# Kernel tuning notes

Measured on AMD Instinct MI355X. Metric: run time of the kernel, lower is better.

The kernel has to match this reference:

```python
import jax, jax.numpy as jnp
import numpy as np

D_MODEL = 1024
N_HEADS = 16
HEAD_DIM = D_MODEL // N_HEADS
SCALE = HEAD_DIM ** -0.5
BATCH = 4
SEQ = 2048


def setup_inputs() -> dict:
    key = jax.random.key(0)
    k_x, k_wqkv, k_bqkv, k_wo, k_bo = jax.random.split(key, 5)
    x = jax.random.normal(k_x, (BATCH, SEQ, D_MODEL), dtype=jnp.float32)
    # causal mask: True = masked (matches torch masked_fill semantics)
    mask = jnp.triu(jnp.ones((SEQ, SEQ), dtype=bool), k=1)
    # Linear params (stored as [in, out] for x @ W)
    lim_qkv = (1.0 / D_MODEL) ** 0.5
    W_qkv = jax.random.uniform(k_wqkv, (D_MODEL, 3 * D_MODEL), jnp.float32, -lim_qkv, lim_qkv)
    b_qkv = jax.random.uniform(k_bqkv, (3 * D_MODEL,), jnp.float32, -lim_qkv, lim_qkv)
    W_out = jax.random.uniform(k_wo, (D_MODEL, D_MODEL), jnp.float32, -lim_qkv, lim_qkv)
    b_out = jax.random.uniform(k_bo, (D_MODEL,), jnp.float32, -lim_qkv, lim_qkv)
    return {"x": x, "mask": mask, "W_qkv": W_qkv, "b_qkv": b_qkv, "W_out": W_out, "b_out": b_out}


def reference(x, mask, W_qkv, b_qkv, W_out, b_out):
    b, s, d = x.shape
    qkv = x @ W_qkv + b_qkv                      # [b, s, 3d]
    qkv = qkv.reshape(b, s, 3, N_HEADS, HEAD_DIM)
    qkv = jnp.transpose(qkv, (2, 0, 3, 1, 4))    # [3, b, h, s, hd]
    q, k, v = qkv[0], qkv[1], qkv[2]
    scores = jnp.einsum('bhqd,bhkd->bhqk', q, k) * SCALE  # [b, h, s, s]
    scores = jnp.where(mask[None, None, :, :], -jnp.inf, scores)
    weights = jax.nn.softmax(scores, axis=-1)
    out = jnp.einsum('bhqk,bhkd->bhqd', weights, v)       # [b, h, s, hd]
    out = jnp.transpose(out, (0, 2, 1, 3)).reshape(b, s, d)
    return out @ W_out + b_out
```

## Files before the change

### kernel.cpp

```cpp
#include <hip/hip_runtime.h>

#define BATCH 4
#define SEQ 2048
#define DM 1024
#define NH 16
#define SCALE 0.125f

typedef unsigned short ushort_t;
typedef short bf16x8 __attribute__((ext_vector_type(8)));
typedef float f32x4 __attribute__((ext_vector_type(4)));

__device__ __forceinline__ ushort_t f2bf(float f) {
    unsigned u = __float_as_uint(f);
    unsigned r = (u + 0x7FFFu + ((u >> 16) & 1u)) >> 16;
    return (ushort_t)r;
}

__device__ __forceinline__ unsigned cvtpk_bf16(float lo, float hi) {
    unsigned r;
    asm("v_cvt_pk_bf16_f32 %0, %1, %2" : "=v"(r) : "v"(lo), "v"(hi));
    return r;
}

__device__ __forceinline__ void glds16(const ushort_t* g, ushort_t* l) {
    __builtin_amdgcn_global_load_lds(
        (const __attribute__((address_space(1))) unsigned*)g,
        (__attribute__((address_space(3))) unsigned*)l, 16, 0, 0);
}

__global__ void cast_f32_bf16(const float* __restrict__ in, ushort_t* __restrict__ out, int n) {
    int i = (blockIdx.x * blockDim.x + threadIdx.x) * 4;
    if (i < n) {
        float4 v = *(const float4*)(in + i);
        ushort4 o;
        o.x = f2bf(v.x); o.y = f2bf(v.y); o.z = f2bf(v.z); o.w = f2bf(v.w);
        *(ushort4*)(out + i) = o;
    }
}

__global__ void transpose_cast(const float* __restrict__ in, ushort_t* __restrict__ out,
                               int K, int N) {
    __shared__ float tile[32][33];
    int n0 = blockIdx.x * 32, k0 = blockIdx.y * 32;
    int x = threadIdx.x, y = threadIdx.y;
#pragma unroll
    for (int j = 0; j < 32; j += 8)
        tile[y + j][x] = in[(size_t)(k0 + y + j) * N + n0 + x];
    __syncthreads();
#pragma unroll
    for (int j = 0; j < 32; j += 8)
        out[(size_t)(n0 + y + j) * K + k0 + x] = f2bf(tile[x][y + j]);
}

template <bool OUT_F32>
__global__ __launch_bounds__(256) void gemm_abt(
    const ushort_t* __restrict__ A, const ushort_t* __restrict__ Bt,
    const float* __restrict__ bias, void* __restrict__ Cout,
    int M, int N, int K) {
    __shared__ __attribute__((aligned(16))) ushort_t As[128 * 64];
    __shared__ __attribute__((aligned(16))) ushort_t Bs[128 * 64];
    const int tid = threadIdx.x;
    const int lane = tid & 63, wave = tid >> 6;
    const int l15 = lane & 15, l4 = lane >> 4;
    const int m0 = blockIdx.y * 128, n0 = blockIdx.x * 128;
    const int wr = (wave >> 1) * 64, wc = (wave & 1) * 64;
    const int r8 = lane >> 3;
    const int kch = (lane & 7) ^ r8;
    const ushort_t* gA = A + (size_t)(m0 + wave * 32 + r8) * K + kch * 8;
    const ushort_t* gB = Bt + (size_t)(n0 + wave * 32 + r8) * K + kch * 8;
    const int r7 = l15 & 7;

    f32x4 acc[4][4];
#pragma unroll
    for (int i = 0; i < 4; ++i)
#pragma unroll
        for (int j = 0; j < 4; ++j) acc[i][j] = (f32x4){0.f, 0.f, 0.f, 0.f};

    for (int k0 = 0; k0 < K; k0 += 64) {
#pragma unroll
        for (int c = 0; c < 4; ++c) {
            glds16(gA + k0 + (size_t)(c * 8) * K, &As[(wave * 32 + c * 8) * 64]);
            glds16(gB + k0 + (size_t)(c * 8) * K, &Bs[(wave * 32 + c * 8) * 64]);
        }
        __syncthreads();
#pragma unroll
        for (int kh = 0; kh < 2; ++kh) {
            const int ch = ((kh * 4 + l4) ^ r7) * 8;
            bf16x8 a[4], b[4];
#pragma unroll
            for (int i = 0; i < 4; ++i) {
                a[i] = *(const bf16x8*)&As[(wr + i * 16 + l15) * 64 + ch];
                b[i] = *(const bf16x8*)&Bs[(wc + i * 16 + l15) * 64 + ch];
            }
#pragma unroll
            for (int mi = 0; mi < 4; ++mi)
#pragma unroll
                for (int ni = 0; ni < 4; ++ni)
                    acc[mi][ni] = __builtin_amdgcn_mfma_f32_16x16x32_bf16(
                        a[mi], b[ni], acc[mi][ni], 0, 0, 0);
        }
        __syncthreads();
    }

#pragma unroll
    for (int mi = 0; mi < 4; ++mi)
#pragma unroll
        for (int ni = 0; ni < 4; ++ni)
#pragma unroll
            for (int r = 0; r < 4; ++r) {
                int row = m0 + wr + mi * 16 + l4 * 4 + r;
                int col = n0 + wc + ni * 16 + l15;
                float v = acc[mi][ni][r] + bias[col];
                if (OUT_F32)
                    ((float*)Cout)[(size_t)row * N + col] = v;
                else
                    ((ushort_t*)Cout)[(size_t)row * N + col] = f2bf(v);
            }
}

struct AState {
    bf16x8 q0, q1;
    f32x4 o[4];
    float m, l;
};

__device__ __forceinline__ void scatterV(ushort_t* V, bf16x8 v0, bf16x8 v1, int key, int d0) {
#pragma unroll
    for (int j = 0; j < 8; ++j) {
        int d = d0 + j;
        V[d * 64 + (key ^ ((d & 7) << 3))] = (ushort_t)v0[j];
        int d2 = d0 + 8 + j;
        V[d2 * 64 + (key ^ ((d2 & 7) << 3))] = (ushort_t)v1[j];
    }
}

#define EXPC 0.18033688011112042f

__device__ __forceinline__ void attn_tile(AState& S, const ushort_t* __restrict__ Ks,
                                          const ushort_t* __restrict__ Vt,
                                          ushort_t* __restrict__ Plw,
                                          int l15, int l4, int rel) {
    float p[16];
    float pmax = -INFINITY;
    __builtin_amdgcn_s_setprio(1);
#pragma unroll
    for (int kt = 0; kt < 4; ++kt) {
        const int row = kt * 16 + l15, r7 = row & 7;
        bf16x8 ak0 = *(const bf16x8*)&Ks[row * 64 + ((l4 ^ r7) * 8)];
        bf16x8 ak1 = *(const bf16x8*)&Ks[row * 64 + (((4 + l4) ^ r7) * 8)];
        f32x4 z = {0.f, 0.f, 0.f, 0.f};
        z = __builtin_amdgcn_mfma_f32_16x16x32_bf16(ak0, S.q0, z, 0, 0, 0);
        z = __builtin_amdgcn_mfma_f32_16x16x32_bf16(ak1, S.q1, z, 0, 0, 0);
#pragma unroll
        for (int r = 0; r < 4; ++r) {
            float v = (kt * 16 + l4 * 4 + r > rel) ? -INFINITY : z[r];
            p[kt * 4 + r] = v;
            pmax = fmaxf(pmax, v);
        }
    }
    __builtin_amdgcn_s_setprio(0);
    pmax = fmaxf(pmax, __shfl_xor(pmax, 16));
    pmax = fmaxf(pmax, __shfl_xor(pmax, 32));

    const bool defer = __all(pmax - S.m <= 64.f);
    const float mref = defer ? S.m : fmaxf(S.m, pmax);
    const float mC = mref * EXPC;
    float rsum = 0.f;
#pragma unroll
    for (int i = 0; i < 16; ++i) {
        p[i] = __builtin_exp2f(fmaf(p[i], EXPC, -mC));
        rsum += p[i];
    }
    rsum += __shfl_xor(rsum, 16);
    rsum += __shfl_xor(rsum, 32);
    if (defer) {
        S.l += rsum;
    } else {
        const float scl = __builtin_exp2f((S.m - mref) * EXPC);
        S.l = S.l * scl + rsum;
        S.m = mref;
        const float sc0 = __shfl(scl, l4 * 4 + 0);
        const float sc1 = __shfl(scl, l4 * 4 + 1);
        const float sc2 = __shfl(scl, l4 * 4 + 2);
        const float sc3 = __shfl(scl, l4 * 4 + 3);
#pragma unroll
        for (int dt = 0; dt < 4; ++dt) {
            S.o[dt][0] *= sc0; S.o[dt][1] *= sc1; S.o[dt][2] *= sc2; S.o[dt][3] *= sc3;
        }
    }

    const int pr7 = l15 & 7;
#pragma unroll
    for (int kt = 0; kt < 4; ++kt) {
        uint2 w;
        w.x = cvtpk_bf16(p[kt * 4 + 0], p[kt * 4 + 1]);
        w.y = cvtpk_bf16(p[kt * 4 + 2], p[kt * 4 + 3]);
        *(uint2*)&Plw[l15 * 64 + ((kt * 16 + l4 * 4) ^ (pr7 << 3))] = w;
    }

    bf16x8 pa0 = *(const bf16x8*)&Plw[l15 * 64 + ((l4 ^ pr7) * 8)];
    bf16x8 pa1 = *(const bf16x8*)&Plw[l15 * 64 + (((4 + l4) ^ pr7) * 8)];
    __builtin_amdgcn_s_setprio(1);
#pragma unroll
    for (int dt = 0; dt < 4; ++dt) {
        const int d = dt * 16 + l15, r7 = d & 7;
        bf16x8 bv0 = *(const bf16x8*)&Vt[d * 64 + ((l4 ^ r7) * 8)];
        bf16x8 bv1 = *(const bf16x8*)&Vt[d * 64 + (((4 + l4) ^ r7) * 8)];
        S.o[dt] = __builtin_amdgcn_mfma_f32_16x16x32_bf16(pa0, bv0, S.o[dt], 0, 0, 0);
        S.o[dt] = __builtin_amdgcn_mfma_f32_16x16x32_bf16(pa1, bv1, S.o[dt], 0, 0, 0);
    }
    __builtin_amdgcn_s_setprio(0);
}

__device__ __forceinline__ void process_qblock(
    int bq, const ushort_t* __restrict__ qkv, ushort_t* __restrict__ out,
    size_t rowbase, int h, int wave, int l15, int l4,
    const ushort_t* gk, const ushort_t* gv, int sv_key, int sv_d0,
    ushort_t* Ks0, ushort_t* Ks1, ushort_t* Vt0, ushort_t* Vt1, ushort_t* Plw) {
    const int qbase = bq * 64 + wave * 16;

    AState S;
    {
        const ushort_t* qp = qkv + (rowbase + qbase + l15) * 3072 + h * 64 + l4 * 8;
        S.q0 = *(const bf16x8*)qp;
        S.q1 = *(const bf16x8*)(qp + 32);
    }
#pragma unroll
    for (int i = 0; i < 4; ++i) S.o[i] = (f32x4){0.f, 0.f, 0.f, 0.f};
    S.m = -INFINITY;
    S.l = 0.f;

    glds16(gk, &Ks0[(wave * 16) * 64]);
    glds16(gk + (size_t)8 * 3072, &Ks0[(wave * 16 + 8) * 64]);
    {
        bf16x8 v0 = *(const bf16x8*)gv;
        bf16x8 v1 = *(const bf16x8*)(gv + 8);
        scatterV(Vt0, v0, v1, sv_key, sv_d0);
    }
    __syncthreads();

    const int nt = bq + 1;
    for (int t = 0; t < nt; ++t) {
        ushort_t* Kc = (t & 1) ? Ks1 : Ks0;
        ushort_t* Vc = (t & 1) ? Vt1 : Vt0;
        ushort_t* Kn = (t & 1) ? Ks0 : Ks1;
        ushort_t* Vn = (t & 1) ? Vt0 : Vt1;
        const bool more = (t + 1 < nt);
        bf16x8 nv0, nv1;
        if (more) {
            const size_t koff = (size_t)(t + 1) * 64 * 3072;
            glds16(gk + koff, &Kn[(wave * 16) * 64]);
            glds16(gk + koff + (size_t)8 * 3072, &Kn[(wave * 16 + 8) * 64]);
            nv0 = *(const bf16x8*)(gv + koff);
            nv1 = *(const bf16x8*)(gv + koff + 8);
        }
        attn_tile(S, Kc, Vc, Plw, l15, l4, qbase + l15 - t * 64);
        if (more)
            scatterV(Vn, nv0, nv1, sv_key, sv_d0);
        __syncthreads();
    }

    const float li0 = __shfl(S.l, l4 * 4 + 0);
    const float li1 = __shfl(S.l, l4 * 4 + 1);
    const float li2 = __shfl(S.l, l4 * 4 + 2);
    const float li3 = __shfl(S.l, l4 * 4 + 3);
#pragma unroll
    for (int r = 0; r < 4; ++r) {
        const int qr = qbase + l4 * 4 + r;
        const float li = (r == 0) ? li0 : (r == 1) ? li1 : (r == 2) ? li2 : li3;
        ushort_t* op = out + (rowbase + qr) * DM + h * 64 + l15;
#pragma unroll
        for (int dt = 0; dt < 4; ++dt)
            op[dt * 16] = f2bf(S.o[dt][r] / li);
    }
}

__global__ __launch_bounds__(256, 4) void attn_kernel(const ushort_t* __restrict__ qkv,
                                                      ushort_t* __restrict__ out) {
    __shared__ __attribute__((aligned(16))) ushort_t Ks[2][64 * 64];
    __shared__ __attribute__((aligned(16))) ushort_t Vt[2][64 * 64];
    __shared__ __attribute__((aligned(16))) ushort_t Pl[4][16 * 64];
    const int tid = threadIdx.x;
    const int wave = tid >> 6, lane = tid & 63;
    const int l15 = lane & 15, l4 = lane >> 4;
    const int bh = blockIdx.x;
    const int b = bh >> 4, h = bh & 15;
    const int pair = blockIdx.y;
    const size_t rowbase = (size_t)b * SEQ;

    const int krow = lane >> 3;
    const int kch = (lane & 7) ^ krow;
    const int sv_key = tid & 63, sv_d0 = (tid >> 6) * 16;
    const ushort_t* gk = qkv + (rowbase + wave * 16 + krow) * 3072 + 1024 + h * 64 + kch * 8;
    const ushort_t* gv = qkv + (rowbase + sv_key) * 3072 + 2048 + h * 64 + sv_d0;

    process_qblock(31 - pair, qkv, out, rowbase, h, wave, l15, l4,
                   gk, gv, sv_key, sv_d0, Ks[0], Ks[1], Vt[0], Vt[1], Pl[wave]);
    process_qblock(pair, qkv, out, rowbase, h, wave, l15, l4,
                   gk, gv, sv_key, sv_d0, Ks[0], Ks[1], Vt[0], Vt[1], Pl[wave]);
}

extern "C" void kernel_launch(void* const* d_in, const int* in_sizes, int n_in,
                              void* d_out, int out_size, void* d_ws, size_t ws_size,
                              hipStream_t stream) {
    const float* x     = (const float*)d_in[0];
    const float* W_qkv = (const float*)d_in[2];
    const float* b_qkv = (const float*)d_in[3];
    const float* W_out = (const float*)d_in[4];
    const float* b_out = (const float*)d_in[5];
    float* out = (float*)d_out;

    char* ws = (char*)d_ws;
    ushort_t* xb    = (ushort_t*)(ws);
    ushort_t* WqkvT = (ushort_t*)(ws + 16777216);
    ushort_t* WoutT = (ushort_t*)(ws + 23068672);
    ushort_t* qkv   = (ushort_t*)(ws + 25165824);
    ushort_t* attn  = (ushort_t*)(ws + 75497472);

    const int nx = BATCH * SEQ * DM;
    cast_f32_bf16<<<nx / (256 * 4), 256, 0, stream>>>(x, xb, nx);
    transpose_cast<<<dim3(3 * DM / 32, DM / 32), dim3(32, 8), 0, stream>>>(W_qkv, WqkvT, DM, 3 * DM);
    transpose_cast<<<dim3(DM / 32, DM / 32), dim3(32, 8), 0, stream>>>(W_out, WoutT, DM, DM);

    gemm_abt<false><<<dim3(3 * DM / 128, BATCH * SEQ / 128), 256, 0, stream>>>(
        xb, WqkvT, b_qkv, qkv, BATCH * SEQ, 3 * DM, DM);

    attn_kernel<<<dim3(BATCH * NH, SEQ / 128), 256, 0, stream>>>(qkv, attn);

    gemm_abt<true><<<dim3(DM / 128, BATCH * SEQ / 128), 256, 0, stream>>>(
        attn, WoutT, b_out, out, BATCH * SEQ, DM, DM);
}
```

Before: 289.8 us.

## Emit transposed V from QKV GEMM epilogue and async-load it in attention

The QKV GEMM now writes Q and K to a packed [tokens, 2048] buffer and V in a per-batch transposed [head_dim, seq] layout straight from its epilogue. The attention kernel can then stage V tiles with the same async global-to-LDS copies used for K, replacing the per-element register scatter into LDS. The causal mask is also specialized so only the diagonal tile pays for the mask compare. The cost is strided 8-byte stores in the V epilogue of the GEMM.

```diff
diff --git a/kernel.cpp b/kernel.cpp
--- a/kernel.cpp
+++ b/kernel.cpp
@@ -52,10 +52,91 @@
         out[(size_t)(n0 + y + j) * K + k0 + x] = f2bf(tile[x][y + j]);
 }
 
-template <bool OUT_F32>
+
+__global__ __launch_bounds__(256) void gemm_qkv(
+    const ushort_t* __restrict__ A, const ushort_t* __restrict__ Bt,
+    const float* __restrict__ bias, ushort_t* __restrict__ qk,
+    ushort_t* __restrict__ vt, int M, int N, int K) {
+    __shared__ __attribute__((aligned(16))) ushort_t As[128 * 64];
+    __shared__ __attribute__((aligned(16))) ushort_t Bs[128 * 64];
+    const int tid = threadIdx.x;
+    const int lane = tid & 63, wave = tid >> 6;
+    const int l15 = lane & 15, l4 = lane >> 4;
+    const int m0 = blockIdx.y * 128, n0 = blockIdx.x * 128;
+    const int wr = (wave >> 1) * 64, wc = (wave & 1) * 64;
+    const int r8 = lane >> 3;
+    const int kch = (lane & 7) ^ r8;
+    const ushort_t* gA = A + (size_t)(m0 + wave * 32 + r8) * K + kch * 8;
+    const ushort_t* gB = Bt + (size_t)(n0 + wave * 32 + r8) * K + kch * 8;
+    const int r7 = l15 & 7;
+
+    f32x4 acc[4][4];
+#pragma unroll
+    for (int i = 0; i < 4; ++i)
+#pragma unroll
+        for (int j = 0; j < 4; ++j) acc[i][j] = (f32x4){0.f, 0.f, 0.f, 0.f};
+
+    for (int k0 = 0; k0 < K; k0 += 64) {
+#pragma unroll
+        for (int c = 0; c < 4; ++c) {
+            glds16(gA + k0 + (size_t)(c * 8) * K, &As[(wave * 32 + c * 8) * 64]);
+            glds16(gB + k0 + (size_t)(c * 8) * K, &Bs[(wave * 32 + c * 8) * 64]);
+        }
+        __syncthreads();
+#pragma unroll
+        for (int kh = 0; kh < 2; ++kh) {
+            const int ch = ((kh * 4 + l4) ^ r7) * 8;
+            bf16x8 a[4], b[4];
+#pragma unroll
+            for (int i = 0; i < 4; ++i) {
+                a[i] = *(const bf16x8*)&As[(wr + i * 16 + l15) * 64 + ch];
+                b[i] = *(const bf16x8*)&Bs[(wc + i * 16 + l15) * 64 + ch];
+            }
+#pragma unroll
+            for (int mi = 0; mi < 4; ++mi)
+#pragma unroll
+                for (int ni = 0; ni < 4; ++ni)
+                    acc[mi][ni] = __builtin_amdgcn_mfma_f32_16x16x32_bf16(
+                        a[mi], b[ni], acc[mi][ni], 0, 0, 0);
+        }
+        __syncthreads();
+    }
+
+    if (n0 < 2048) {
+#pragma unroll
+        for (int mi = 0; mi < 4; ++mi)
+#pragma unroll
+            for (int ni = 0; ni < 4; ++ni) {
+                const int col = n0 + wc + ni * 16 + l15;
+                const float bv = bias[col];
+#pragma unroll
+                for (int r = 0; r < 4; ++r) {
+                    const int row = m0 + wr + mi * 16 + l4 * 4 + r;
+                    qk[(size_t)row * 2048 + col] = f2bf(acc[mi][ni][r] + bv);
+                }
+            }
+    } else {
+#pragma unroll
+        for (int mi = 0; mi < 4; ++mi)
+#pragma unroll
+            for (int ni = 0; ni < 4; ++ni) {
+                const int hdg = n0 + wc + ni * 16 + l15 - 2048;
+                const float bv = bias[2048 + hdg];
+                const int row0 = m0 + wr + mi * 16 + l4 * 4;
+                const int bb = row0 >> 11, s0 = row0 & 2047;
+                ushort4 pk;
+                pk.x = f2bf(acc[mi][ni][0] + bv);
+                pk.y = f2bf(acc[mi][ni][1] + bv);
+                pk.z = f2bf(acc[mi][ni][2] + bv);
+                pk.w = f2bf(acc[mi][ni][3] + bv);
+                *(ushort4*)&vt[((size_t)bb * 1024 + hdg) * 2048 + s0] = pk;
+            }
+    }
+}
+
 __global__ __launch_bounds__(256) void gemm_abt(
     const ushort_t* __restrict__ A, const ushort_t* __restrict__ Bt,
-    const float* __restrict__ bias, void* __restrict__ Cout,
+    const float* __restrict__ bias, float* __restrict__ Cout,
     int M, int N, int K) {
     __shared__ __attribute__((aligned(16))) ushort_t As[128 * 64];
     __shared__ __attribute__((aligned(16))) ushort_t Bs[128 * 64];
@@ -108,13 +189,9 @@
         for (int ni = 0; ni < 4; ++ni)
 #pragma unroll
             for (int r = 0; r < 4; ++r) {
-                int row = m0 + wr + mi * 16 + l4 * 4 + r;
-                int col = n0 + wc + ni * 16 + l15;
-                float v = acc[mi][ni][r] + bias[col];
-                if (OUT_F32)
-                    ((float*)Cout)[(size_t)row * N + col] = v;
-                else
-                    ((ushort_t*)Cout)[(size_t)row * N + col] = f2bf(v);
+                const int row = m0 + wr + mi * 16 + l4 * 4 + r;
+                const int col = n0 + wc + ni * 16 + l15;
+                Cout[(size_t)row * N + col] = acc[mi][ni][r] + bias[col];
             }
 }
 
@@ -124,18 +201,9 @@
     float m, l;
 };
 
-__device__ __forceinline__ void scatterV(ushort_t* V, bf16x8 v0, bf16x8 v1, int key, int d0) {
-#pragma unroll
-    for (int j = 0; j < 8; ++j) {
-        int d = d0 + j;
-        V[d * 64 + (key ^ ((d & 7) << 3))] = (ushort_t)v0[j];
-        int d2 = d0 + 8 + j;
-        V[d2 * 64 + (key ^ ((d2 & 7) << 3))] = (ushort_t)v1[j];
-    }
-}
-
 #define EXPC 0.18033688011112042f
 
+template <bool MASK>
 __device__ __forceinline__ void attn_tile(AState& S, const ushort_t* __restrict__ Ks,
                                           const ushort_t* __restrict__ Vt,
                                           ushort_t* __restrict__ Plw,
@@ -153,7 +221,8 @@
         z = __builtin_amdgcn_mfma_f32_16x16x32_bf16(ak1, S.q1, z, 0, 0, 0);
 #pragma unroll
         for (int r = 0; r < 4; ++r) {
-            float v = (kt * 16 + l4 * 4 + r > rel) ? -INFINITY : z[r];
+            float v = z[r];
+            if (MASK) v = (kt * 16 + l4 * 4 + r > rel) ? -INFINITY : v;
             p[kt * 4 + r] = v;
             pmax = fmaxf(pmax, v);
         }
@@ -213,15 +282,15 @@
 }
 
 __device__ __forceinline__ void process_qblock(
-    int bq, const ushort_t* __restrict__ qkv, ushort_t* __restrict__ out,
+    int bq, const ushort_t* __restrict__ qk, ushort_t* __restrict__ out,
     size_t rowbase, int h, int wave, int l15, int l4,
-    const ushort_t* gk, const ushort_t* gv, int sv_key, int sv_d0,
+    const ushort_t* gk, const ushort_t* gvt,
     ushort_t* Ks0, ushort_t* Ks1, ushort_t* Vt0, ushort_t* Vt1, ushort_t* Plw) {
     const int qbase = bq * 64 + wave * 16;
 
     AState S;
     {
-        const ushort_t* qp = qkv + (rowbase + qbase + l15) * 3072 + h * 64 + l4 * 8;
+        const ushort_t* qp = qk + (rowbase + qbase + l15) * 2048 + h * 64 + l4 * 8;
         S.q0 = *(const bf16x8*)qp;
         S.q1 = *(const bf16x8*)(qp + 32);
     }
@@ -231,12 +300,9 @@
     S.l = 0.f;
 
     glds16(gk, &Ks0[(wave * 16) * 64]);
-    glds16(gk + (size_t)8 * 3072, &Ks0[(wave * 16 + 8) * 64]);
-    {
-        bf16x8 v0 = *(const bf16x8*)gv;
-        bf16x8 v1 = *(const bf16x8*)(gv + 8);
-        scatterV(Vt0, v0, v1, sv_key, sv_d0);
-    }
+    glds16(gk + (size_t)8 * 2048, &Ks0[(wave * 16 + 8) * 64]);
+    glds16(gvt, &Vt0[(wave * 16) * 64]);
+    glds16(gvt + (size_t)8 * 2048, &Vt0[(wave * 16 + 8) * 64]);
     __syncthreads();
 
     const int nt = bq + 1;
@@ -245,18 +311,18 @@
         ushort_t* Vc = (t & 1) ? Vt1 : Vt0;
         ushort_t* Kn = (t & 1) ? Ks0 : Ks1;
         ushort_t* Vn = (t & 1) ? Vt0 : Vt1;
-        const bool more = (t + 1 < nt);
-        bf16x8 nv0, nv1;
-        if (more) {
-            const size_t koff = (size_t)(t + 1) * 64 * 3072;
+        if (t + 1 < nt) {
+            const size_t koff = (size_t)(t + 1) * 64 * 2048;
             glds16(gk + koff, &Kn[(wave * 16) * 64]);
-            glds16(gk + koff + (size_t)8 * 3072, &Kn[(wave * 16 + 8) * 64]);
-            nv0 = *(const bf16x8*)(gv + koff);
-            nv1 = *(const bf16x8*)(gv + koff + 8);
-        }
-        attn_tile(S, Kc, Vc, Plw, l15, l4, qbase + l15 - t * 64);
-        if (more)
-            scatterV(Vn, nv0, nv1, sv_key, sv_d0);
+            glds16(gk + koff + (size_t)8 * 2048, &Kn[(wave * 16 + 8) * 64]);
+            const size_t voff = (size_t)(t + 1) * 64;
+            glds16(gvt + voff, &Vn[(wave * 16) * 64]);
+            glds16(gvt + voff + (size_t)8 * 2048, &Vn[(wave * 16 + 8) * 64]);
+        }
+        if (t == bq)
+            attn_tile<true>(S, Kc, Vc, Plw, l15, l4, wave * 16 + l15);
+        else
+            attn_tile<false>(S, Kc, Vc, Plw, l15, l4, 0);
         __syncthreads();
     }
 
@@ -275,7 +341,8 @@
     }
 }
 
-__global__ __launch_bounds__(256, 4) void attn_kernel(const ushort_t* __restrict__ qkv,
+__global__ __launch_bounds__(256, 4) void attn_kernel(const ushort_t* __restrict__ qk,
+                                                      const ushort_t* __restrict__ vt,
                                                       ushort_t* __restrict__ out) {
     __shared__ __attribute__((aligned(16))) ushort_t Ks[2][64 * 64];
     __shared__ __attribute__((aligned(16))) ushort_t Vt[2][64 * 64];
@@ -290,14 +357,13 @@
 
     const int krow = lane >> 3;
     const int kch = (lane & 7) ^ krow;
-    const int sv_key = tid & 63, sv_d0 = (tid >> 6) * 16;
-    const ushort_t* gk = qkv + (rowbase + wave * 16 + krow) * 3072 + 1024 + h * 64 + kch * 8;
-    const ushort_t* gv = qkv + (rowbase + sv_key) * 3072 + 2048 + h * 64 + sv_d0;
-
-    process_qblock(31 - pair, qkv, out, rowbase, h, wave, l15, l4,
-                   gk, gv, sv_key, sv_d0, Ks[0], Ks[1], Vt[0], Vt[1], Pl[wave]);
-    process_qblock(pair, qkv, out, rowbase, h, wave, l15, l4,
-                   gk, gv, sv_key, sv_d0, Ks[0], Ks[1], Vt[0], Vt[1], Pl[wave]);
+    const ushort_t* gk = qk + (rowbase + wave * 16 + krow) * 2048 + 1024 + h * 64 + kch * 8;
+    const ushort_t* gvt = vt + ((size_t)b * 1024 + h * 64 + wave * 16 + krow) * 2048 + kch * 8;
+
+    process_qblock(31 - pair, qk, out, rowbase, h, wave, l15, l4,
+                   gk, gvt, Ks[0], Ks[1], Vt[0], Vt[1], Pl[wave]);
+    process_qblock(pair, qk, out, rowbase, h, wave, l15, l4,
+                   gk, gvt, Ks[0], Ks[1], Vt[0], Vt[1], Pl[wave]);
 }
 
 extern "C" void kernel_launch(void* const* d_in, const int* in_sizes, int n_in,
@@ -314,7 +380,8 @@
     ushort_t* xb    = (ushort_t*)(ws);
     ushort_t* WqkvT = (ushort_t*)(ws + 16777216);
     ushort_t* WoutT = (ushort_t*)(ws + 23068672);
-    ushort_t* qkv   = (ushort_t*)(ws + 25165824);
+    ushort_t* qk    = (ushort_t*)(ws + 25165824);
+    ushort_t* vt    = (ushort_t*)(ws + 58720256);
     ushort_t* attn  = (ushort_t*)(ws + 75497472);
 
     const int nx = BATCH * SEQ * DM;
@@ -322,11 +389,11 @@
     transpose_cast<<<dim3(3 * DM / 32, DM / 32), dim3(32, 8), 0, stream>>>(W_qkv, WqkvT, DM, 3 * DM);
     transpose_cast<<<dim3(DM / 32, DM / 32), dim3(32, 8), 0, stream>>>(W_out, WoutT, DM, DM);
 
-    gemm_abt<false><<<dim3(3 * DM / 128, BATCH * SEQ / 128), 256, 0, stream>>>(
-        xb, WqkvT, b_qkv, qkv, BATCH * SEQ, 3 * DM, DM);
-
-    attn_kernel<<<dim3(BATCH * NH, SEQ / 128), 256, 0, stream>>>(qkv, attn);
-
-    gemm_abt<true><<<dim3(DM / 128, BATCH * SEQ / 128), 256, 0, stream>>>(
+    gemm_qkv<<<dim3(3 * DM / 128, BATCH * SEQ / 128), 256, 0, stream>>>(
+        xb, WqkvT, b_qkv, qk, vt, BATCH * SEQ, 3 * DM, DM);
+
+    attn_kernel<<<dim3(BATCH * NH, SEQ / 128), 256, 0, stream>>>(qk, vt, attn);
+
+    gemm_abt<<<dim3(DM / 128, BATCH * SEQ / 128), 256, 0, stream>>>(
         attn, WoutT, b_out, out, BATCH * SEQ, DM, DM);
 }
```

New measurement: 286.8 us. About the same (-1.0%).
